# Performance work log

Measured on AMD Instinct MI355X. Metric: run time of the kernel, lower is better.

Reference implementation:

```python
import jax, jax.numpy as jnp
import numpy as np

N_NODES = 50000
N_EDGES = 800000
NODE_DIM = 128
EDGE_DIM = 64
HIDDEN = 256


def setup_inputs() -> dict:
    key = jax.random.key(0)
    ks = jax.random.split(key, 12)
    glorot = lambda k, fi, fo: jax.random.normal(k, (fi, fo), jnp.float32) * (2.0 / (fi + fo)) ** 0.5
    return {
        "node_features": jax.random.normal(ks[0], (N_NODES, NODE_DIM), jnp.float32),
        "edge_features": jax.random.normal(ks[1], (N_EDGES, EDGE_DIM), jnp.float32),
        "src": jax.random.randint(ks[2], (N_EDGES,), 0, N_NODES),
        "dst": jax.random.randint(ks[3], (N_EDGES,), 0, N_NODES),
        # edge_update MLP: (2*node_dim + edge_dim) -> hidden -> edge_dim
        "We1": glorot(ks[4], 2 * NODE_DIM + EDGE_DIM, HIDDEN),
        "be1": jnp.zeros((HIDDEN,), jnp.float32),
        "We2": glorot(ks[5], HIDDEN, EDGE_DIM),
        "be2": jnp.zeros((EDGE_DIM,), jnp.float32),
        # node_update MLP: (node_dim + edge_dim) -> hidden -> node_dim
        "Wn1": glorot(ks[6], NODE_DIM + EDGE_DIM, HIDDEN),
        "bn1": jnp.zeros((HIDDEN,), jnp.float32),
        "Wn2": glorot(ks[7], HIDDEN, NODE_DIM),
        "bn2": jnp.zeros((NODE_DIM,), jnp.float32),
    }


def reference(node_features, edge_features, src, dst, We1, be1, We2, be2, Wn1, bn1, Wn2, bn2):
    # message: per-edge MLP on [src_h, e, dst_h]
    concat = jnp.concatenate(
        [node_features[src], edge_features, node_features[dst]], axis=1
    )  # [E, 2*node_dim + edge_dim]
    e_upd = jax.nn.relu(concat @ We1 + be1) @ We2 + be2  # [E, edge_dim]

    # reduce: sum incoming messages per destination node
    e_sum = jax.ops.segment_sum(e_upd, dst, num_segments=node_features.shape[0])  # [N, edge_dim]
    node_in = jnp.concatenate([node_features, e_sum], axis=1)  # [N, node_dim + edge_dim]
    h_new = jax.nn.relu(node_in @ Wn1 + bn1) @ Wn2 + bn2  # [N, node_dim]

    # DGL only applies reduce_func to nodes with at least one incoming edge
    deg = jax.ops.segment_sum(jnp.ones_like(dst, jnp.float32), dst, num_segments=node_features.shape[0])
    h_out = jnp.where(deg[:, None] > 0, h_new, node_features)

    # original module never writes e_updated back: returned edge features are the inputs
    return h_out, edge_features
```

## Files before the change

kernel.cpp:

```cpp
#include <hip/hip_runtime.h>

#define N_NODES 50000
#define N_EDGES 800000
#define NODE_DIM 128
#define EDGE_DIM 64
#define HIDDEN 256
#define K_N 192

typedef __attribute__((ext_vector_type(8))) short bf16x8;
typedef __attribute__((ext_vector_type(4))) float f32x4;
typedef __attribute__((ext_vector_type(16))) float f32x16;
typedef unsigned short u16;
typedef unsigned int u32;

#define MFMA16 __builtin_amdgcn_mfma_f32_16x16x32_bf16
#define MFMA32 __builtin_amdgcn_mfma_f32_32x32x16_bf16

__device__ inline u16 f2bf(float f) {
  u32 u = __builtin_bit_cast(u32, f);
  u += 0x7fffu + ((u >> 16) & 1u);
  return (u16)(u >> 16);
}
__device__ inline float bf2f(u16 u) {
  u32 x = ((u32)u) << 16;
  return __builtin_bit_cast(float, x);
}
__device__ inline u32 cvt_pk(float a, float b) {
  u32 r;
  asm("v_cvt_pk_bf16_f32 %0, %1, %2" : "=v"(r) : "v"(a), "v"(b));
  return r;
}
__device__ inline void st_bf4(u16* p, float4 v) {
  ushort4 r;
  r.x = f2bf(v.x); r.y = f2bf(v.y); r.z = f2bf(v.z); r.w = f2bf(v.w);
  *reinterpret_cast<ushort4*>(p) = r;
}

template<bool EFB>
__global__ __launch_bounds__(256) void convert_kernel(
    const float* __restrict__ ef, float* __restrict__ out_edge,
    u16* __restrict__ efb_edge) {
  const int stride = gridDim.x * blockDim.x;
  const float4* s = reinterpret_cast<const float4*>(ef);
  float4* o = reinterpret_cast<float4*>(out_edge);
  uint2* b = reinterpret_cast<uint2*>(efb_edge);
  for (int g = blockIdx.x * blockDim.x + threadIdx.x;
       g < N_EDGES * 16; g += stride) {
    float4 v = s[g];
    o[g] = v;
    if (EFB) {
      uint2 r;
      r.x = cvt_pk(v.x, v.y);
      r.y = cvt_pk(v.z, v.w);
      b[g] = r;
    }
  }
}

__global__ void prep_weights(const float* __restrict__ We1, const float* __restrict__ We2,
                             const float* __restrict__ Wn1, const float* __restrict__ Wn2,
                             const float* __restrict__ be2, const int* __restrict__ dst,
                             u16* __restrict__ w1st, u16* __restrict__ w1dt,
                             u16* __restrict__ w1ef, u16* __restrict__ w2y,
                             u16* __restrict__ wn1t, u16* __restrict__ wn2t,
                             float* __restrict__ b2p, int* __restrict__ hist) {
  const int stride = gridDim.x * blockDim.x;
  const int tid = blockIdx.x * blockDim.x + threadIdx.x;
  for (int i = tid; i < HIDDEN * NODE_DIM; i += stride) {
    int h = i >> 7, k = i & 127;
    w1st[i] = f2bf(We1[k * HIDDEN + h]);
    w1dt[i] = f2bf(We1[(192 + k) * HIDDEN + h]);
  }
  for (int i = tid; i < 8 * 4 * 64 * 8; i += stride) {
    int jj = i & 7;
    int l = (i >> 3) & 63;
    int kb = (i >> 9) & 3;
    int ht = i >> 11;
    int h = ht * 32 + (l & 31);
    int kloc = kb * 16 + (l >> 5) * 8 + jj;
    w1ef[i] = f2bf(We1[(128 + kloc) * HIDDEN + h]);
  }
  for (int i = tid; i < EDGE_DIM * HIDDEN; i += stride) {
    int jj = i & 7;
    int l = (i >> 3) & 63;
    int t2 = (i >> 9) & 1;
    int kb2 = i >> 10;
    int out = t2 * 32 + (l & 31);
    int hi = l >> 5;
    int k = kb2 * 16 + (jj & 3) + 8 * (jj >> 2) + 4 * hi;
    w2y[i] = f2bf(We2[k * EDGE_DIM + out]);
  }
  for (int i = tid; i < HIDDEN * K_N; i += stride) {
    int n = i / K_N, k = i % K_N;
    wn1t[i] = f2bf(Wn1[k * HIDDEN + n]);
  }
  for (int i = tid; i < NODE_DIM * HIDDEN; i += stride) {
    int n = i / HIDDEN, k = i % HIDDEN;
    wn2t[i] = f2bf(Wn2[k * NODE_DIM + n]);
  }
  for (int i = tid; i < EDGE_DIM; i += stride) {
    int t2 = i >> 5, hi = (i >> 4) & 1, r = i & 15;
    b2p[i] = be2[t2 * 32 + (r & 3) + 8 * (r >> 2) + 4 * hi];
  }
  for (int i = tid; i < N_EDGES; i += stride)
    atomicAdd(&hist[dst[i]], 1);
}

#define NB_P 782
#define SA_P 136
#define SH   264

__global__ __launch_bounds__(256) void pgemm_kernel(
    const float* __restrict__ nf, const u16* __restrict__ w1st,
    const u16* __restrict__ w1dt, const float* __restrict__ be1,
    u16* __restrict__ P_src, u16* __restrict__ P_dst)
{
  __shared__ u16 A[64 * SA_P];
  __shared__ u16 H[64 * SH];
  const int tid = threadIdx.x;
  const int n0 = blockIdx.x * 64;
  const float4* nf4 = reinterpret_cast<const float4*>(nf);

  #pragma unroll
  for (int p = 0; p < 8; ++p) {
    int i = p * 256 + tid;
    int row = i >> 5, c4 = i & 31;
    int rg = min(n0 + row, N_NODES - 1);
    float4 v = nf4[(size_t)rg * 32 + c4];
    st_bf4(&A[row * SA_P + c4 * 4], v);
  }
  __syncthreads();

  const int wave = tid >> 6, lane = tid & 63;
  const int lr = lane & 15;
  const int lk = (lane >> 4) * 8;

  for (int table = 0; table < 2; ++table) {
    const u16* w = table ? w1dt : w1st;
    u16* P = table ? P_dst : P_src;

    f32x4 acc[4][4] = {};
    #pragma unroll
    for (int kb = 0; kb < 4; ++kb) {
      const int ko = kb * 32 + lk;
      bf16x8 a[4], bb[4];
      #pragma unroll
      for (int mt = 0; mt < 4; ++mt)
        a[mt] = *reinterpret_cast<const bf16x8*>(&A[(mt * 16 + lr) * SA_P + ko]);
      #pragma unroll
      for (int nt = 0; nt < 4; ++nt)
        bb[nt] = *reinterpret_cast<const bf16x8*>(&w[(size_t)(wave * 64 + nt * 16 + lr) * 128 + ko]);
      #pragma unroll
      for (int mt = 0; mt < 4; ++mt)
        #pragma unroll
        for (int nt = 0; nt < 4; ++nt)
          acc[mt][nt] = MFMA16(a[mt], bb[nt], acc[mt][nt], 0, 0, 0);
    }
    __syncthreads();

    #pragma unroll
    for (int mt = 0; mt < 4; ++mt)
      #pragma unroll
      for (int nt = 0; nt < 4; ++nt) {
        int col = wave * 64 + nt * 16 + lr;
        float bias = table ? 0.f : be1[col];
        #pragma unroll
        for (int j = 0; j < 4; ++j) {
          int row = mt * 16 + (lane >> 4) * 4 + j;
          H[row * SH + col] = f2bf(acc[mt][nt][j] + bias);
        }
      }
    __syncthreads();

    #pragma unroll
    for (int p = 0; p < 16; ++p) {
      int u = p * 256 + tid;
      int row = u >> 6, cg = u & 63;
      int hi = cg >> 5, ht = (cg >> 2) & 7, q = cg & 3;
      int hbase = ht * 32 + 8 * q + 4 * hi;
      int n = n0 + row;
      if (n < N_NODES) {
        ushort4 v = *reinterpret_cast<const ushort4*>(&H[row * SH + hbase]);
        *reinterpret_cast<ushort4*>(&P[(size_t)n * 256 + cg * 4]) = v;
      }
    }
  }
}

#define NB_SCAN 196

__global__ void scanA_kernel(const int* __restrict__ hist, int* __restrict__ eid) {
  __shared__ int red[256];
  int gid = blockIdx.x * 256 + threadIdx.x;
  int v = (gid < N_NODES) ? hist[gid] : 0;
  red[threadIdx.x] = v;
  __syncthreads();
  for (int d = 128; d > 0; d >>= 1) {
    if (threadIdx.x < d) red[threadIdx.x] += red[threadIdx.x + d];
    __syncthreads();
  }
  if (threadIdx.x == 0) eid[blockIdx.x] = red[0];
}

__global__ void scanB_kernel(int* __restrict__ eid, int* __restrict__ off) {
  __shared__ int ssum[256];
  int tid = threadIdx.x;
  int v = (tid < NB_SCAN) ? eid[tid] : 0;
  ssum[tid] = v;
  __syncthreads();
  for (int d = 1; d < 256; d <<= 1) {
    int t = (tid >= d) ? ssum[tid - d] : 0;
    __syncthreads();
    ssum[tid] += t;
    __syncthreads();
  }
  if (tid < NB_SCAN) eid[256 + tid] = ssum[tid] - v;
  if (tid == 255) off[N_NODES] = ssum[255];
}

__global__ void scanC_kernel(const int* __restrict__ hist, const int* __restrict__ eid,
                             int* __restrict__ off, int* __restrict__ cursor,
                             float* __restrict__ e_sum) {
  __shared__ int ssum[256];
  int tid = threadIdx.x;
  int gid = blockIdx.x * 256 + tid;
  int base = eid[256 + blockIdx.x];
  int v = (gid < N_NODES) ? hist[gid] : 0;
  ssum[tid] = v;
  __syncthreads();
  for (int d = 1; d < 256; d <<= 1) {
    int t = (tid >= d) ? ssum[tid - d] : 0;
    __syncthreads();
    ssum[tid] += t;
    __syncthreads();
  }
  if (gid < N_NODES) {
    int o = base + ssum[tid] - v;
    off[gid] = o;
    cursor[gid] = o;
    float4 z = {0.f, 0.f, 0.f, 0.f};
    float4* ez = reinterpret_cast<float4*>(e_sum + (size_t)gid * 64);
    #pragma unroll
    for (int q = 0; q < 16; ++q) ez[q] = z;
  }
}

__global__ void scatter_kernel(const int* __restrict__ src, const int* __restrict__ dst,
                               int* __restrict__ cursor, int* __restrict__ eid,
                               int* __restrict__ csr_src, int* __restrict__ csr_dst) {
  int e = blockIdx.x * blockDim.x + threadIdx.x;
  if (e < N_EDGES) {
    int d = dst[e];
    int pos = atomicAdd(&cursor[d], 1);
    eid[pos] = e;
    csr_src[pos] = src[e];
    csr_dst[pos] = d;
  }
}

template<bool EFB>
__global__ __launch_bounds__(256, 4) void edge_mlp(
    const u16* __restrict__ P_src, const u16* __restrict__ P_dst,
    const float* __restrict__ ef, const u16* __restrict__ efb_edge,
    const int* __restrict__ eid, const int* __restrict__ csr_src,
    const int* __restrict__ csr_dst,
    const u16* __restrict__ w1ef, const u16* __restrict__ w2y,
    const float* __restrict__ b2p,
    float* __restrict__ e_sum)
{
  __shared__ char shmem[33280];
  u16* W1e = reinterpret_cast<u16*>(shmem);
  float* bounce = reinterpret_cast<float*>(shmem);

  const int tid = threadIdx.x;
  const int wv = tid >> 6, lane = tid & 63;
  const int ecol = lane & 31;
  const int hi = lane >> 5;
  const int e0 = blockIdx.x * 128;
  const int pos = e0 + wv * 32 + ecol;

  {
    const uint4* s = reinterpret_cast<const uint4*>(w1ef);
    uint4* d = reinterpret_cast<uint4*>(W1e);
    #pragma unroll
    for (int j = 0; j < 8; ++j) d[j * 256 + tid] = s[j * 256 + tid];
  }

  const int e    = eid[pos];
  const int srcn = csr_src[pos];
  const int dstn = csr_dst[pos];

  bf16x8 efr[4];
  if (EFB) {
    const u16* eb = efb_edge + (size_t)e * 64 + hi * 8;
    #pragma unroll
    for (int kb = 0; kb < 4; ++kb)
      efr[kb] = *reinterpret_cast<const bf16x8*>(eb + kb * 16);
  } else {
    #pragma unroll
    for (int kb = 0; kb < 4; ++kb) {
      const float* ep = ef + (size_t)e * 64 + kb * 16 + hi * 8;
      float4 lo = *reinterpret_cast<const float4*>(ep);
      float4 hv = *reinterpret_cast<const float4*>(ep + 4);
      u32 w[4];
      w[0] = cvt_pk(lo.x, lo.y); w[1] = cvt_pk(lo.z, lo.w);
      w[2] = cvt_pk(hv.x, hv.y); w[3] = cvt_pk(hv.z, hv.w);
      efr[kb] = __builtin_bit_cast(bf16x8, *reinterpret_cast<uint4*>(w));
    }
  }

  __syncthreads();

  f32x16 acc2[2];
  #pragma unroll
  for (int t2 = 0; t2 < 2; ++t2) {
    const float* bp = b2p + t2 * 32 + hi * 16;
    #pragma unroll
    for (int r = 0; r < 16; ++r) acc2[t2][r] = bp[r];
  }

  const u16* psb = P_src + (size_t)srcn * 256 + hi * 128;
  const u16* pdb = P_dst + (size_t)dstn * 256 + hi * 128;

  bf16x8 pa0 = *reinterpret_cast<const bf16x8*>(psb);
  bf16x8 pa1 = *reinterpret_cast<const bf16x8*>(psb + 8);
  bf16x8 pd0 = *reinterpret_cast<const bf16x8*>(pdb);
  bf16x8 pd1 = *reinterpret_cast<const bf16x8*>(pdb + 8);

  #pragma unroll
  for (int ht = 0; ht < 8; ++ht) {
    bf16x8 na0, na1, nd0, nd1;
    if (ht < 7) {
      na0 = *reinterpret_cast<const bf16x8*>(psb + (ht + 1) * 16);
      na1 = *reinterpret_cast<const bf16x8*>(psb + (ht + 1) * 16 + 8);
      nd0 = *reinterpret_cast<const bf16x8*>(pdb + (ht + 1) * 16);
      nd1 = *reinterpret_cast<const bf16x8*>(pdb + (ht + 1) * 16 + 8);
    }

    f32x16 acc;
    #pragma unroll
    for (int r = 0; r < 8; ++r) {
      acc[r]     = bf2f((u16)pa0[r]) + bf2f((u16)pd0[r]);
      acc[8 + r] = bf2f((u16)pa1[r]) + bf2f((u16)pd1[r]);
    }

    #pragma unroll
    for (int kb = 0; kb < 4; ++kb) {
      bf16x8 wf = *reinterpret_cast<const bf16x8*>(W1e + ((ht * 4 + kb) * 64 + lane) * 8);
      acc = MFMA32(wf, efr[kb], acc, 0, 0, 0);
    }

    #pragma unroll
    for (int s2 = 0; s2 < 2; ++s2) {
      bf16x8 hf;
      u32* hw = reinterpret_cast<u32*>(&hf);
      #pragma unroll
      for (int m = 0; m < 4; ++m)
        hw[m] = cvt_pk(fmaxf(acc[s2 * 8 + 2 * m], 0.f),
                       fmaxf(acc[s2 * 8 + 2 * m + 1], 0.f));
      #pragma unroll
      for (int t2 = 0; t2 < 2; ++t2) {
        bf16x8 wf2 = *reinterpret_cast<const bf16x8*>(
            w2y + ((size_t)((ht * 2 + s2) * 2 + t2) * 64 + lane) * 8);
        acc2[t2] = MFMA32(wf2, hf, acc2[t2], 0, 0, 0);
      }
    }

    pa0 = na0; pa1 = na1; pd0 = nd0; pd1 = nd1;
  }

  __syncthreads();

  {
    const int lp = wv * 32 + ecol;
    #pragma unroll
    for (int t2 = 0; t2 < 2; ++t2)
      #pragma unroll
      for (int r = 0; r < 16; ++r) {
        int o = t2 * 32 + (r & 3) + 8 * (r >> 2) + 4 * hi;
        bounce[lp * 65 + o] = acc2[t2][r];
      }
  }

  {
    const int d = lane;
    const int base = wv * 32;
    float s = bounce[base * 65 + d];
    int cur = __shfl(dstn, 0, 64);
    #pragma unroll 4
    for (int i = 1; i < 32; ++i) {
      int nx = __shfl(dstn, i, 64);
      float v = bounce[(base + i) * 65 + d];
      if (nx == cur) {
        s += v;
      } else {
        atomicAdd(&e_sum[(size_t)cur * 64 + d], s);
        cur = nx;
        s = v;
      }
    }
    atomicAdd(&e_sum[(size_t)cur * 64 + d], s);
  }
}

#define SA_N 200

__global__ __launch_bounds__(256) void node_kernel(
    const float* __restrict__ nf, const float* __restrict__ e_sum,
    const int* __restrict__ hist,
    const u16* __restrict__ w1, const float* __restrict__ b1,
    const u16* __restrict__ w2, const float* __restrict__ b2,
    float* __restrict__ hout)
{
  __shared__ u16 A[64 * SH];
  const int tid = threadIdx.x;
  const int n0 = blockIdx.x * 64;

  const float4* nf4 = reinterpret_cast<const float4*>(nf);
  const float4* es4 = reinterpret_cast<const float4*>(e_sum);

  #pragma unroll
  for (int p = 0; p < 8; ++p) {
    int i = p * 256 + tid;
    int row = i >> 5, c4 = i & 31;
    int rg = min(n0 + row, N_NODES - 1);
    float4 v = nf4[(size_t)rg * 32 + c4];
    st_bf4(&A[row * SA_N + c4 * 4], v);
  }
  #pragma unroll
  for (int p = 0; p < 4; ++p) {
    int i = p * 256 + tid;
    int row = i >> 4, c4 = i & 15;
    int rg = min(n0 + row, N_NODES - 1);
    float4 v = es4[(size_t)rg * 16 + c4];
    st_bf4(&A[row * SA_N + 128 + c4 * 4], v);
  }
  __syncthreads();

  const int wave = tid >> 6, lane = tid & 63;
  const int lr = lane & 15;
  const int lk = (lane >> 4) * 8;

  f32x4 acc[4][4] = {};
  for (int kb = 0; kb < K_N / 32; ++kb) {
    const int ko = kb * 32 + lk;
    bf16x8 a[4], b[4];
    #pragma unroll
    for (int mt = 0; mt < 4; ++mt)
      a[mt] = *reinterpret_cast<const bf16x8*>(&A[(mt * 16 + lr) * SA_N + ko]);
    #pragma unroll
    for (int nt = 0; nt < 4; ++nt)
      b[nt] = *reinterpret_cast<const bf16x8*>(&w1[(size_t)(wave * 64 + nt * 16 + lr) * K_N + ko]);
    #pragma unroll
    for (int mt = 0; mt < 4; ++mt)
      #pragma unroll
      for (int nt = 0; nt < 4; ++nt)
        acc[mt][nt] = MFMA16(a[mt], b[nt], acc[mt][nt], 0, 0, 0);
  }
  __syncthreads();

  u16* H = A;
  #pragma unroll
  for (int mt = 0; mt < 4; ++mt)
    #pragma unroll
    for (int nt = 0; nt < 4; ++nt) {
      int col = wave * 64 + nt * 16 + lr;
      float bias = b1[col];
      #pragma unroll
      for (int j = 0; j < 4; ++j) {
        int row = mt * 16 + (lane >> 4) * 4 + j;
        float h = acc[mt][nt][j] + bias;
        H[row * SH + col] = f2bf(h > 0.f ? h : 0.f);
      }
    }
  __syncthreads();

  f32x4 acc2[8] = {};
  for (int kb = 0; kb < HIDDEN / 32; ++kb) {
    const int ko = kb * 32 + lk;
    bf16x8 a = *reinterpret_cast<const bf16x8*>(&H[(wave * 16 + lr) * SH + ko]);
    #pragma unroll
    for (int nt = 0; nt < 8; ++nt) {
      bf16x8 b = *reinterpret_cast<const bf16x8*>(&w2[(size_t)(nt * 16 + lr) * HIDDEN + ko]);
      acc2[nt] = MFMA16(a, b, acc2[nt], 0, 0, 0);
    }
  }
  #pragma unroll
  for (int nt = 0; nt < 8; ++nt) {
    int col = nt * 16 + lr;
    float bias = b2[col];
    #pragma unroll
    for (int j = 0; j < 4; ++j) {
      int row = wave * 16 + (lane >> 4) * 4 + j;
      int rg = n0 + row;
      if (rg < N_NODES) {
        float v = acc2[nt][j] + bias;
        hout[(size_t)rg * NODE_DIM + col] =
            (hist[rg] != 0) ? v : nf[(size_t)rg * NODE_DIM + col];
      }
    }
  }
}

extern "C" void kernel_launch(void* const* d_in, const int* in_sizes, int n_in,
                              void* d_out, int out_size, void* d_ws, size_t ws_size,
                              hipStream_t stream) {
  const float* nf  = (const float*)d_in[0];
  const float* ef  = (const float*)d_in[1];
  const int*   src = (const int*)d_in[2];
  const int*   dst = (const int*)d_in[3];
  const float* We1 = (const float*)d_in[4];
  const float* be1 = (const float*)d_in[5];
  const float* We2 = (const float*)d_in[6];
  const float* be2 = (const float*)d_in[7];
  const float* Wn1 = (const float*)d_in[8];
  const float* bn1 = (const float*)d_in[9];
  const float* Wn2 = (const float*)d_in[10];
  const float* bn2 = (const float*)d_in[11];

  float* hout = (float*)d_out;
  float* out_edge = hout + (size_t)N_NODES * NODE_DIM;

  char* ws = (char*)d_ws;
  int*   hist    = (int*)ws;
  int*   off     = (int*)(ws + 200000);
  int*   cursor  = (int*)(ws + 400016);
  int*   eid     = (int*)(ws + 600016);
  int*   csr_src = (int*)(ws + 3800016);
  int*   csr_dst = (int*)(ws + 7000016);
  float* e_sum   = (float*)(ws + 10200016);
  u16*   w1ef    = (u16*)(ws + 23000016);
  u16*   w1st    = (u16*)(ws + 23032784);
  u16*   w1dt    = (u16*)(ws + 23098320);
  u16*   w2y     = (u16*)(ws + 23163856);
  u16*   wn1t    = (u16*)(ws + 23196624);
  u16*   wn2t    = (u16*)(ws + 23294928);
  float* b2p     = (float*)(ws + 23360464);
  u16*   P_src   = (u16*)(ws + 23360720);
  u16*   P_dst   = (u16*)(ws + 48960720);
  u16*   efb_edge= (u16*)(ws + 74560720);
  const size_t NEED_EFB = 176960720;
  const int efb = (ws_size >= NEED_EFB) ? 1 : 0;

  hipMemsetAsync(hist, 0, 200000, stream);
  prep_weights<<<512, 256, 0, stream>>>(We1, We2, Wn1, Wn2, be2, dst,
                                        w1st, w1dt, w1ef, w2y, wn1t, wn2t,
                                        b2p, hist);
  if (efb) convert_kernel<true><<<2048, 256, 0, stream>>>(ef, out_edge, efb_edge);
  else     convert_kernel<false><<<2048, 256, 0, stream>>>(ef, out_edge, efb_edge);
  pgemm_kernel<<<NB_P, 256, 0, stream>>>(nf, w1st, w1dt, be1, P_src, P_dst);
  scanA_kernel<<<NB_SCAN, 256, 0, stream>>>(hist, eid);
  scanB_kernel<<<1, 256, 0, stream>>>(eid, off);
  scanC_kernel<<<NB_SCAN, 256, 0, stream>>>(hist, eid, off, cursor, e_sum);
  scatter_kernel<<<(N_EDGES + 255) / 256, 256, 0, stream>>>(src, dst, cursor, eid,
                                                            csr_src, csr_dst);
  if (efb) {
    edge_mlp<true><<<N_EDGES / 128, 256, 0, stream>>>(
        P_src, P_dst, ef, efb_edge, eid, csr_src, csr_dst,
        w1ef, w2y, b2p, e_sum);
  } else {
    edge_mlp<false><<<N_EDGES / 128, 256, 0, stream>>>(
        P_src, P_dst, ef, efb_edge, eid, csr_src, csr_dst,
        w1ef, w2y, b2p, e_sum);
  }
  node_kernel<<<(N_NODES + 63) / 64, 256, 0, stream>>>(nf, e_sum, hist,
                                                       wn1t, bn1, wn2t, bn2, hout);
}
```

Before: 512.5 us.

## Fuse edge-feature copy into scatter kernel and double-buffer P loads in edge MLP

Removes the separate convert kernel and moves the edge-feature copy and bf16 conversion into the scatter kernel as a grid-stride loop, saving one launch and letting the memory-bound copy overlap with the atomic scatter. In the edge MLP, the gathered P_src/P_dst rows are now prefetched two hidden tiles ahead in a two-slot buffer instead of one, to hide gather latency. This costs more registers, which could lower occupancy at the 4-blocks launch bound, and the scatter kernel becomes heavier per thread.

```diff
diff --git a/kernel.cpp b/kernel.cpp
--- a/kernel.cpp
+++ b/kernel.cpp
@@ -34,27 +34,6 @@
   ushort4 r;
   r.x = f2bf(v.x); r.y = f2bf(v.y); r.z = f2bf(v.z); r.w = f2bf(v.w);
   *reinterpret_cast<ushort4*>(p) = r;
-}
-
-template<bool EFB>
-__global__ __launch_bounds__(256) void convert_kernel(
-    const float* __restrict__ ef, float* __restrict__ out_edge,
-    u16* __restrict__ efb_edge) {
-  const int stride = gridDim.x * blockDim.x;
-  const float4* s = reinterpret_cast<const float4*>(ef);
-  float4* o = reinterpret_cast<float4*>(out_edge);
-  uint2* b = reinterpret_cast<uint2*>(efb_edge);
-  for (int g = blockIdx.x * blockDim.x + threadIdx.x;
-       g < N_EDGES * 16; g += stride) {
-    float4 v = s[g];
-    o[g] = v;
-    if (EFB) {
-      uint2 r;
-      r.x = cvt_pk(v.x, v.y);
-      r.y = cvt_pk(v.z, v.w);
-      b[g] = r;
-    }
-  }
 }
 
 __global__ void prep_weights(const float* __restrict__ We1, const float* __restrict__ We2,
@@ -245,16 +224,34 @@
   }
 }
 
-__global__ void scatter_kernel(const int* __restrict__ src, const int* __restrict__ dst,
-                               int* __restrict__ cursor, int* __restrict__ eid,
-                               int* __restrict__ csr_src, int* __restrict__ csr_dst) {
-  int e = blockIdx.x * blockDim.x + threadIdx.x;
-  if (e < N_EDGES) {
-    int d = dst[e];
+template<bool EFB>
+__global__ __launch_bounds__(256) void scatter_kernel(
+    const int* __restrict__ src, const int* __restrict__ dst,
+    const float* __restrict__ ef, float* __restrict__ out_edge,
+    u16* __restrict__ efb_edge,
+    int* __restrict__ cursor, int* __restrict__ eid,
+    int* __restrict__ csr_src, int* __restrict__ csr_dst) {
+  const int gtid = blockIdx.x * blockDim.x + threadIdx.x;
+  if (gtid < N_EDGES) {
+    int d = dst[gtid];
     int pos = atomicAdd(&cursor[d], 1);
-    eid[pos] = e;
-    csr_src[pos] = src[e];
+    eid[pos] = gtid;
+    csr_src[pos] = src[gtid];
     csr_dst[pos] = d;
+  }
+  const int stride = gridDim.x * blockDim.x;
+  const float4* s = reinterpret_cast<const float4*>(ef);
+  float4* o = reinterpret_cast<float4*>(out_edge);
+  uint2* b = reinterpret_cast<uint2*>(efb_edge);
+  for (int g = gtid; g < N_EDGES * 16; g += stride) {
+    float4 v = s[g];
+    o[g] = v;
+    if (EFB) {
+      uint2 r;
+      r.x = cvt_pk(v.x, v.y);
+      r.y = cvt_pk(v.z, v.w);
+      b[g] = r;
+    }
   }
 }
 
@@ -322,26 +319,31 @@
   const u16* psb = P_src + (size_t)srcn * 256 + hi * 128;
   const u16* pdb = P_dst + (size_t)dstn * 256 + hi * 128;
 
-  bf16x8 pa0 = *reinterpret_cast<const bf16x8*>(psb);
-  bf16x8 pa1 = *reinterpret_cast<const bf16x8*>(psb + 8);
-  bf16x8 pd0 = *reinterpret_cast<const bf16x8*>(pdb);
-  bf16x8 pd1 = *reinterpret_cast<const bf16x8*>(pdb + 8);
+  bf16x8 ps[2][2], pd[2][2];
+  #pragma unroll
+  for (int st = 0; st < 2; ++st) {
+    ps[st][0] = *reinterpret_cast<const bf16x8*>(psb + st * 16);
+    ps[st][1] = *reinterpret_cast<const bf16x8*>(psb + st * 16 + 8);
+    pd[st][0] = *reinterpret_cast<const bf16x8*>(pdb + st * 16);
+    pd[st][1] = *reinterpret_cast<const bf16x8*>(pdb + st * 16 + 8);
+  }
 
   #pragma unroll
   for (int ht = 0; ht < 8; ++ht) {
-    bf16x8 na0, na1, nd0, nd1;
-    if (ht < 7) {
-      na0 = *reinterpret_cast<const bf16x8*>(psb + (ht + 1) * 16);
-      na1 = *reinterpret_cast<const bf16x8*>(psb + (ht + 1) * 16 + 8);
-      nd0 = *reinterpret_cast<const bf16x8*>(pdb + (ht + 1) * 16);
-      nd1 = *reinterpret_cast<const bf16x8*>(pdb + (ht + 1) * 16 + 8);
-    }
+    const int st = ht & 1;
 
     f32x16 acc;
     #pragma unroll
     for (int r = 0; r < 8; ++r) {
-      acc[r]     = bf2f((u16)pa0[r]) + bf2f((u16)pd0[r]);
-      acc[8 + r] = bf2f((u16)pa1[r]) + bf2f((u16)pd1[r]);
+      acc[r]     = bf2f((u16)ps[st][0][r]) + bf2f((u16)pd[st][0][r]);
+      acc[8 + r] = bf2f((u16)ps[st][1][r]) + bf2f((u16)pd[st][1][r]);
+    }
+
+    if (ht + 2 < 8) {
+      ps[st][0] = *reinterpret_cast<const bf16x8*>(psb + (ht + 2) * 16);
+      ps[st][1] = *reinterpret_cast<const bf16x8*>(psb + (ht + 2) * 16 + 8);
+      pd[st][0] = *reinterpret_cast<const bf16x8*>(pdb + (ht + 2) * 16);
+      pd[st][1] = *reinterpret_cast<const bf16x8*>(pdb + (ht + 2) * 16 + 8);
     }
 
     #pragma unroll
@@ -365,8 +367,6 @@
         acc2[t2] = MFMA32(wf2, hf, acc2[t2], 0, 0, 0);
       }
     }
-
-    pa0 = na0; pa1 = na1; pd0 = nd0; pd1 = nd1;
   }
 
   __syncthreads();
@@ -546,19 +546,19 @@
   prep_weights<<<512, 256, 0, stream>>>(We1, We2, Wn1, Wn2, be2, dst,
                                         w1st, w1dt, w1ef, w2y, wn1t, wn2t,
                                         b2p, hist);
-  if (efb) convert_kernel<true><<<2048, 256, 0, stream>>>(ef, out_edge, efb_edge);
-  else     convert_kernel<false><<<2048, 256, 0, stream>>>(ef, out_edge, efb_edge);
   pgemm_kernel<<<NB_P, 256, 0, stream>>>(nf, w1st, w1dt, be1, P_src, P_dst);
   scanA_kernel<<<NB_SCAN, 256, 0, stream>>>(hist, eid);
   scanB_kernel<<<1, 256, 0, stream>>>(eid, off);
   scanC_kernel<<<NB_SCAN, 256, 0, stream>>>(hist, eid, off, cursor, e_sum);
-  scatter_kernel<<<(N_EDGES + 255) / 256, 256, 0, stream>>>(src, dst, cursor, eid,
-                                                            csr_src, csr_dst);
   if (efb) {
+    scatter_kernel<true><<<(N_EDGES + 255) / 256, 256, 0, stream>>>(
+        src, dst, ef, out_edge, efb_edge, cursor, eid, csr_src, csr_dst);
     edge_mlp<true><<<N_EDGES / 128, 256, 0, stream>>>(
         P_src, P_dst, ef, efb_edge, eid, csr_src, csr_dst,
         w1ef, w2y, b2p, e_sum);
   } else {
+    scatter_kernel<false><<<(N_EDGES + 255) / 256, 256, 0, stream>>>(
+        src, dst, ef, out_edge, efb_edge, cursor, eid, csr_src, csr_dst);
     edge_mlp<false><<<N_EDGES / 128, 256, 0, stream>>>(
         P_src, P_dst, ef, efb_edge, eid, csr_src, csr_dst,
         w1ef, w2y, b2p, e_sum);
```

Result: no change. 515.5 us (+0.6%).
